# Optimization experiments

Hardware: AMD Instinct MI355X
Metric: run time of the kernel (lower is better)

The kernel has to match this reference:

```python
import jax, jax.numpy as jnp
import numpy as np

EPS = 1e-6

def _mlp3(x, Wa, ba, Wb, bb, Wc, bc):
    h = jax.nn.relu(x @ Wa + ba)
    h = jax.nn.relu(h @ Wb + bb)
    return h @ Wc + bc

def setup_inputs() -> dict:
    key = jax.random.key(0)
    ks = jax.random.split(key, 16)
    B, D, C, N = 1024, 1024, 128, 100000
    s = 0.02  # weight scale
    return {
        "query": jax.random.normal(ks[0], (B, D), jnp.float32),
        "W1": jax.random.normal(ks[1], (D, D // 2), jnp.float32) * s,
        "b1": jnp.zeros((D // 2,), jnp.float32),
        "W2": jax.random.normal(ks[2], (D // 2, D // 4), jnp.float32) * s,
        "b2": jnp.zeros((D // 4,), jnp.float32),
        "W3": jax.random.normal(ks[3], (D // 4, C), jnp.float32) * s,
        "b3": jnp.zeros((C,), jnp.float32),
        "keys": jax.random.normal(ks[4], (N, C), jnp.float32),
        "values": jax.random.normal(ks[5], (N, C), jnp.float32),
        "D1w": jax.random.normal(ks[6], (C, D // 4), jnp.float32) * s,
        "D1b": jnp.zeros((D // 4,), jnp.float32),
        "D2w": jax.random.normal(ks[7], (D // 4, D // 2), jnp.float32) * s,
        "D2b": jnp.zeros((D // 2,), jnp.float32),
        "D3w": jax.random.normal(ks[8], (D // 2, D), jnp.float32) * s,
        "D3b": jnp.zeros((D,), jnp.float32),
        "k": 5,
    }

def reference(query, W1, b1, W2, b2, W3, b3, keys, values,
              D1w, D1b, D2w, D2b, D3w, D3b, k):
    # Compress query (FAISS path detaches, so stop_gradient is faithful)
    cq = _mlp3(query, W1, b1, W2, b2, W3, b3)          # [B, C]
    cq = jax.lax.stop_gradient(cq)
    keys_c = jax.lax.stop_gradient(keys)
    vals = jax.lax.stop_gradient(values)               # stored values were .detach()ed
    # Brute-force squared-L2 distances (IndexFlatL2 returns squared L2): [B, N]
    d2 = (jnp.sum(cq * cq, axis=1, keepdims=True)
          + jnp.sum(keys_c * keys_c, axis=1)[None, :]
          - 2.0 * cq @ keys_c.T)
    neg_d, idx = jax.lax.top_k(-d2, k)                 # k nearest, ascending distance
    dist = -neg_d                                      # [B, k]
    w = 1.0 / (dist + EPS)
    w = w / jnp.sum(w, axis=1, keepdims=True)          # [B, k]
    gathered = vals[idx]                               # [B, k, C]
    weighted = jnp.einsum('bk,bkc->bc', w, gathered)   # [B, C]
    retrieved = _mlp3(weighted, D1w, D1b, D2w, D2b, D3w, D3b)  # [B, D]
    confidence = 1.0 / (dist[:, 0] + EPS)              # [B]
    return retrieved, confidence
```

## Files before the change

### kernel.cpp

```cpp
#include <hip/hip_runtime.h>
#include <hip/hip_bf16.h>

#define NKEYS  100000
#define NCH    192
#define CHK    576
#define TPC    9
#define KPAD   (NCH * CHK)
#define NTILE  (KPAD / 64)
#define BQ     1024
#define EPS_F  1e-6f
#define NCAND  (NCH * 3)
#define BIGF   1e30f

typedef __attribute__((ext_vector_type(8))) short bf16x8;
typedef __attribute__((ext_vector_type(4))) float f32x4;

__device__ __forceinline__ void gl_lds16(const uint4* g, uint4* l) {
    __builtin_amdgcn_global_load_lds((const __attribute__((address_space(1))) void*)g,
                                     (__attribute__((address_space(3))) void*)l, 16, 0, 0);
}
__device__ __forceinline__ unsigned umn(unsigned a, unsigned b) { return a < b ? a : b; }
__device__ __forceinline__ unsigned umx(unsigned a, unsigned b) { return a > b ? a : b; }
__device__ __forceinline__ ushort bf16bits(float v) {
    __hip_bfloat16 h = __float2bfloat16(v);
    return *(ushort*)&h;
}

__device__ __forceinline__ void ins3u(unsigned (&m)[3], unsigned u) {
    unsigned v1 = umn(m[2], u);
    m[2] = umx(m[1], v1);
    unsigned v2 = umn(m[1], v1);
    m[1] = umx(m[0], v2);
    m[0] = umn(m[0], v2);
}

__device__ __forceinline__ void ins5(float (&d)[5], int (&ix)[5], float nd, int ni) {
    if (nd < d[4]) {
        d[4] = nd; ix[4] = ni;
#pragma unroll
        for (int p = 4; p > 0; --p) {
            if (d[p] < d[p - 1]) {
                float td = d[p]; d[p] = d[p - 1]; d[p - 1] = td;
                int   ti = ix[p]; ix[p] = ix[p - 1]; ix[p - 1] = ti;
            }
        }
    }
}

__global__ __launch_bounds__(256)
void cvt_keys(const float* __restrict__ keys, uint4* __restrict__ img,
              float* __restrict__ kk, float* __restrict__ khalf) {
    const int tid = threadIdx.x;
    const int r = tid >> 2, s = tid & 3;
    const int tile = blockIdx.x;
    const int n = tile * 64 + r;
    const int ct = r >> 4, l15 = r & 15;
    const bool live = (n < NKEYS);
    const float* kp = keys + (size_t)n * 128 + s * 32;
    float ss = 0.f;
    uint4 out[4];
#pragma unroll
    for (int q = 0; q < 4; ++q) {
        float4 a = make_float4(0.f, 0.f, 0.f, 0.f), b = a;
        if (live) { a = *(const float4*)(kp + q * 8); b = *(const float4*)(kp + q * 8 + 4); }
        ss += a.x * a.x + a.y * a.y + a.z * a.z + a.w * a.w
            + b.x * b.x + b.y * b.y + b.z * b.z + b.w * b.w;
        float v[8] = {a.x, a.y, a.z, a.w, b.x, b.y, b.z, b.w};
        ushort h[8];
#pragma unroll
        for (int j = 0; j < 8; ++j) h[j] = bf16bits(v[j]);
        out[q] = make_uint4((uint)h[0] | ((uint)h[1] << 16), (uint)h[2] | ((uint)h[3] << 16),
                            (uint)h[4] | ((uint)h[5] << 16), (uint)h[6] | ((uint)h[7] << 16));
    }
    ss += __shfl_xor(ss, 1, 64);
    ss += __shfl_xor(ss, 2, 64);
    if (s == 0) {
        kk[n]    = live ? ss : BIGF;
        khalf[n] = live ? -0.5f * ss : -BIGF;
    }
#pragma unroll
    for (int q = 0; q < 4; ++q)
        img[(size_t)tile * 1024 + ((ct * 4 + s) * 4 + q) * 16 + l15] = out[q];
}

__global__ __launch_bounds__(256)
void prep(const float* __restrict__ A, ushort* __restrict__ Ax,
          const float* __restrict__ W, uint4* __restrict__ Wimg) {
    const int b = blockIdx.x;
    if (b < 1024) {
        const int row = b;
        const int i = threadIdx.x * 4;
        float4 v = *(const float4*)&A[(size_t)row * 1024 + i];
        float x[4] = {v.x, v.y, v.z, v.w};
        ushort h[4], l[4];
#pragma unroll
        for (int j = 0; j < 4; ++j) {
            __hip_bfloat16 hb = __float2bfloat16(x[j]);
            h[j] = *(ushort*)&hb;
            l[j] = bf16bits(x[j] - __bfloat162float(hb));
        }
        ushort* o = Ax + (size_t)row * 3072;
        *(ushort4*)&o[i]        = make_ushort4(h[0], h[1], h[2], h[3]);
        *(ushort4*)&o[1024 + i] = make_ushort4(l[0], l[1], l[2], l[3]);
        *(ushort4*)&o[2048 + i] = make_ushort4(h[0], h[1], h[2], h[3]);
    } else {
        const int idx = b - 1024;
        const int ctile = idx / 48, p = idx % 48;
        const int part = p >> 4, psrc = p & 15;
#pragma unroll
        for (int it = 0; it < 2; ++it) {
            int c = it * 256 + threadIdx.x;
            int l15 = c & 15, quad = (c >> 4) & 3, s = (c >> 6) & 1, ct = c >> 7;
            int n = ctile * 64 + ct * 16 + l15;
            int k = psrc * 64 + s * 32 + quad * 8;
            ushort h[8];
#pragma unroll
            for (int j = 0; j < 8; ++j) {
                float w = W[(size_t)(k + j) * 512 + n];
                __hip_bfloat16 hb = __float2bfloat16(w);
                if (part < 2) h[j] = *(ushort*)&hb;
                else h[j] = bf16bits(w - __bfloat162float(hb));
            }
            Wimg[((size_t)ctile * 48 + p) * 512 + c] =
                make_uint4((uint)h[0] | ((uint)h[1] << 16), (uint)h[2] | ((uint)h[3] << 16),
                           (uint)h[4] | ((uint)h[5] << 16), (uint)h[6] | ((uint)h[7] << 16));
        }
    }
}

__global__ __launch_bounds__(256)
void bgemm_part(const ushort* __restrict__ Abf, const uint4* __restrict__ Wimg,
                float* __restrict__ P, int M, int N, int K, int ppz) {
    __shared__ uint4 pan[2][512];
    const int tid = threadIdx.x;
    const int wv = tid >> 6, ln = tid & 63;
    const int quad = ln >> 4, l15 = ln & 15;
    const int n0 = blockIdx.x * 64;
    const int m0 = blockIdx.y * 128 + wv * 32;
    const int ctile = blockIdx.x, npanT = K >> 6;
    const int p0 = blockIdx.z * ppz;
    f32x4 acc[2][4];
#pragma unroll
    for (int s = 0; s < 2; ++s)
#pragma unroll
        for (int c = 0; c < 4; ++c) acc[s][c] = (f32x4){0.f, 0.f, 0.f, 0.f};

#pragma unroll
    for (int it = 0; it < 2; ++it)
        gl_lds16(&Wimg[((size_t)ctile * npanT + p0) * 512 + it * 256 + wv * 64 + ln],
                 &pan[0][it * 256 + wv * 64]);
    __syncthreads();

    for (int pp = 0; pp < ppz; ++pp) {
        const int p = p0 + pp;
        const int b = pp & 1;
        if (pp + 1 < ppz) {
#pragma unroll
            for (int it = 0; it < 2; ++it)
                gl_lds16(&Wimg[((size_t)ctile * npanT + p + 1) * 512 + it * 256 + wv * 64 + ln],
                         &pan[b ^ 1][it * 256 + wv * 64]);
        }
        const ushort* arow = Abf + (size_t)(m0 + l15) * K + p * 64 + quad * 8;
        bf16x8 afA[2], afB[2];
#pragma unroll
        for (int s = 0; s < 2; ++s) {
            afA[s] = *(const bf16x8*)(arow + s * 32);
            afB[s] = *(const bf16x8*)(arow + (size_t)16 * K + s * 32);
        }
#pragma unroll
        for (int ct = 0; ct < 4; ++ct)
#pragma unroll
            for (int s = 0; s < 2; ++s) {
                bf16x8 bfr = *(const bf16x8*)&pan[b][((ct * 2 + s) * 4 + quad) * 16 + l15];
                acc[0][ct] = __builtin_amdgcn_mfma_f32_16x16x32_bf16(afA[s], bfr, acc[0][ct], 0, 0, 0);
                acc[1][ct] = __builtin_amdgcn_mfma_f32_16x16x32_bf16(afB[s], bfr, acc[1][ct], 0, 0, 0);
            }
        __syncthreads();
    }

    P += (size_t)blockIdx.z * M * N;
#pragma unroll
    for (int ct = 0; ct < 4; ++ct) {
        const int col = n0 + ct * 16 + l15;
#pragma unroll
        for (int set = 0; set < 2; ++set)
#pragma unroll
            for (int r = 0; r < 4; ++r)
                P[(size_t)(m0 + set * 16 + quad * 4 + r) * N + col] = acc[set][ct][r];
    }
}

template <int NP>
__global__ __launch_bounds__(256)
void sgemm_part(const float* __restrict__ A, const float* __restrict__ abias,
                const float* __restrict__ W, float* __restrict__ P,
                int M, int N, int K, int kslice, int MNpart) {
    __shared__ float As[16][68];
    __shared__ float Bs[16][64];
    const int tid = threadIdx.x;
    const int tx = tid & 15, ty = tid >> 4;
    const int m0 = blockIdx.y * 64, n0 = blockIdx.x * 64;
    const int kb = blockIdx.z * kslice, ke = kb + kslice;
    float acc[4][4] = {};
    for (int k0 = kb; k0 < ke; k0 += 16) {
        {
            int m = tid >> 2, k4 = (tid & 3) * 4;
            const float* ap = &A[(size_t)(m0 + m) * K + k0 + k4];
            float4 a = *(const float4*)ap;
            if (NP > 0) {
#pragma unroll
                for (int z = 1; z < NP; ++z) {
                    float4 v = *(const float4*)(ap + (size_t)z * MNpart);
                    a.x += v.x; a.y += v.y; a.z += v.z; a.w += v.w;
                }
                float4 b = *(const float4*)&abias[k0 + k4];
                a.x = fmaxf(a.x + b.x, 0.f); a.y = fmaxf(a.y + b.y, 0.f);
                a.z = fmaxf(a.z + b.z, 0.f); a.w = fmaxf(a.w + b.w, 0.f);
            }
            As[k4 + 0][m] = a.x; As[k4 + 1][m] = a.y;
            As[k4 + 2][m] = a.z; As[k4 + 3][m] = a.w;
        }
        {
            int k = tid >> 4, n4 = (tid & 15) * 4;
            *(float4*)&Bs[k][n4] = *(const float4*)&W[(size_t)(k0 + k) * N + n0 + n4];
        }
        __syncthreads();
#pragma unroll
        for (int kkk = 0; kkk < 16; ++kkk) {
            float4 a4 = *(const float4*)&As[kkk][ty * 4];
            float4 b4 = *(const float4*)&Bs[kkk][tx * 4];
            float av[4] = {a4.x, a4.y, a4.z, a4.w};
            float bv[4] = {b4.x, b4.y, b4.z, b4.w};
#pragma unroll
            for (int i = 0; i < 4; ++i)
#pragma unroll
                for (int j = 0; j < 4; ++j)
                    acc[i][j] = fmaf(av[i], bv[j], acc[i][j]);
        }
        __syncthreads();
    }
    P += (size_t)blockIdx.z * M * N;
#pragma unroll
    for (int i = 0; i < 4; ++i)
        *(float4*)&P[(size_t)(m0 + ty * 4 + i) * N + n0 + tx * 4] =
            make_float4(acc[i][0], acc[i][1], acc[i][2], acc[i][3]);
}

__global__ __launch_bounds__(128)
void final_row(const float* __restrict__ P, const float* __restrict__ bias,
               float* __restrict__ cq, ushort* __restrict__ qbf,
               float* __restrict__ qq) {
    __shared__ float red[2];
    const int row = blockIdx.x, c = threadIdx.x;
    float v = 0.f;
#pragma unroll
    for (int z = 0; z < 4; ++z) v += P[(size_t)z * (BQ * 128) + row * 128 + c];
    v += bias[c];
    cq[(size_t)row * 128 + c] = v;
    qbf[(size_t)row * 128 + c] = bf16bits(v);
    float s = v * v;
#pragma unroll
    for (int off = 32; off > 0; off >>= 1) s += __shfl_down(s, off, 64);
    if ((c & 63) == 0) red[c >> 6] = s;
    __syncthreads();
    if (c == 0) qq[row] = red[0] + red[1];
}

__device__ __forceinline__ void wT_panel(const float* __restrict__ W, uint4* __restrict__ Wimg,
                                         int K, int N, int ctile, int p) {
    const int npan = K >> 6;
#pragma unroll
    for (int it = 0; it < 2; ++it) {
        int c = it * 256 + threadIdx.x;
        int l15 = c & 15, quad = (c >> 4) & 3, s = (c >> 6) & 1, ct = c >> 7;
        int n = ctile * 64 + ct * 16 + l15;
        int k = p * 64 + s * 32 + quad * 8;
        ushort h[8];
#pragma unroll
        for (int j = 0; j < 8; ++j) h[j] = bf16bits(W[(size_t)(k + j) * N + n]);
        Wimg[((size_t)ctile * npan + p) * 512 + c] =
            make_uint4((uint)h[0] | ((uint)h[1] << 16), (uint)h[2] | ((uint)h[3] << 16),
                       (uint)h[4] | ((uint)h[5] << 16), (uint)h[6] | ((uint)h[7] << 16));
    }
}

__global__ __launch_bounds__(256)
void cvt_wT_all(const float* __restrict__ W1, const float* __restrict__ W2,
                const float* __restrict__ W3, uint4* __restrict__ I1,
                uint4* __restrict__ I2, uint4* __restrict__ I3) {
    int b = blockIdx.x;
    if (b < 8)       { wT_panel(W1, I1, 128, 256,  b >> 1, b & 1); }
    else if (b < 40) { b -= 8;  wT_panel(W2, I2, 256, 512,  b >> 2, b & 3); }
    else             { b -= 40; wT_panel(W3, I3, 512, 1024, b >> 3, b & 7); }
}

__global__ __launch_bounds__(512, 4)
void screen_topk(const ushort* __restrict__ qbf, const uint4* __restrict__ img,
                 const float* __restrict__ khalf, int* __restrict__ cand_i) {
    __shared__ uint4 buf[2][1024];
    __shared__ float kls[CHK];
    const int tid = threadIdx.x;
    const int wv = tid >> 6, ln = tid & 63;
    const int quad = ln >> 4, l15 = ln & 15;
    const int m0 = blockIdx.y * 256 + wv * 32;
    const int c0 = blockIdx.x * CHK;
    const int t0 = blockIdx.x * TPC;

    bf16x8 afA[4], afB[4];
    {
        const ushort* qa = qbf + (size_t)(m0 + l15) * 128 + quad * 8;
#pragma unroll
        for (int s = 0; s < 4; ++s) {
            afA[s] = *(const bf16x8*)(qa + 32 * s);
            afB[s] = *(const bf16x8*)(qa + 16 * 128 + 32 * s);
        }
    }
    for (int i = tid; i < CHK; i += 512) kls[i] = khalf[c0 + i];

    unsigned mA[4][3], mB[4][3];
#pragma unroll
    for (int r = 0; r < 4; ++r)
#pragma unroll
        for (int p = 0; p < 3; ++p) { mA[r][p] = 0xFFFFFFFFu; mB[r][p] = 0xFFFFFFFFu; }

#pragma unroll
    for (int it = 0; it < 2; ++it)
        gl_lds16(&img[(size_t)t0 * 1024 + it * 512 + wv * 64 + ln],
                 &buf[0][it * 512 + wv * 64]);
    __syncthreads();

    for (int t = 0; t < TPC; ++t) {
        const int b = t & 1;
        if (t + 1 < TPC) {
#pragma unroll
            for (int it = 0; it < 2; ++it)
                gl_lds16(&img[(size_t)(t0 + t + 1) * 1024 + it * 512 + wv * 64 + ln],
                         &buf[b ^ 1][it * 512 + wv * 64]);
        }
#pragma unroll
        for (int ct = 0; ct < 4; ++ct) {
            const int nl = t * 64 + ct * 16 + l15;
            const float kh = kls[nl];
            f32x4 a0 = {kh, kh, kh, kh}, a1 = {kh, kh, kh, kh};
#pragma unroll
            for (int s = 0; s < 4; ++s) {
                bf16x8 bfr = *(const bf16x8*)&buf[b][(ct * 4 + s) * 64 + ln];
                a0 = __builtin_amdgcn_mfma_f32_16x16x32_bf16(afA[s], bfr, a0, 0, 0, 0);
                a1 = __builtin_amdgcn_mfma_f32_16x16x32_bf16(afB[s], bfr, a1, 0, 0, 0);
            }
#pragma unroll
            for (int r = 0; r < 4; ++r) {
                ins3u(mA[r], (__float_as_uint(a0[r]) & 0xFFFFF800u) | (unsigned)nl);
                ins3u(mB[r], (__float_as_uint(a1[r]) & 0xFFFFF800u) | (unsigned)nl);
            }
        }
        __syncthreads();
    }

#pragma unroll
    for (int set = 0; set < 2; ++set) {
#pragma unroll
        for (int r = 0; r < 4; ++r) {
            unsigned m[3];
#pragma unroll
            for (int p = 0; p < 3; ++p) m[p] = set ? mB[r][p] : mA[r][p];
#pragma unroll
            for (int st = 1; st <= 8; st <<= 1) {
                unsigned o[3];
#pragma unroll
                for (int p = 0; p < 3; ++p) o[p] = (unsigned)__shfl_xor((int)m[p], st, 64);
#pragma unroll
                for (int p = 0; p < 3; ++p) ins3u(m, o[p]);
            }
            if (l15 == 0) {
                const int row = m0 + set * 16 + quad * 4 + r;
#pragma unroll
                for (int p = 0; p < 3; ++p)
                    cand_i[((size_t)row * NCH + blockIdx.x) * 3 + p] = c0 + (int)(m[p] & 0x7FFu);
            }
        }
    }
}

__global__ __launch_bounds__(512)
void rerank_gather(const int* __restrict__ cand_i, const float* __restrict__ cq,
                   const float* __restrict__ keysf, const float* __restrict__ qq,
                   const float* __restrict__ kk, const float* __restrict__ values,
                   ushort* __restrict__ wbf, float* __restrict__ conf_out) {
    __shared__ __align__(16) float qs[128];
    __shared__ float ed[NCAND];
    __shared__ int   ei[NCAND];
    __shared__ float w5[5];
    __shared__ int   s5[5];
    __shared__ float confs;
    const int row = blockIdx.x, tid = threadIdx.x;
    const int ln = tid & 63;
    const int qd = tid >> 4;
    const int l15 = tid & 15;
    if (tid < 128) qs[tid] = cq[(size_t)row * 128 + tid];
    for (int c = tid; c < NCAND; c += 512) ei[c] = cand_i[(size_t)row * NCAND + c];
    __syncthreads();
    const float4 qa = *(const float4*)&qs[l15 * 8];
    const float4 qb = *(const float4*)&qs[l15 * 8 + 4];
    const float qqr = qq[row];
#pragma unroll 3
    for (int it = 0; it < (NCAND + 31) / 32; ++it) {
        const int c = qd + it * 32;
        if (c < NCAND) {
            const int idx = ei[c];
            const int idc = idx < NKEYS ? idx : NKEYS - 1;
            const float* kp = &keysf[(size_t)idc * 128 + l15 * 8];
            const float4 ka = *(const float4*)kp;
            const float4 kb = *(const float4*)(kp + 4);
            float dot = qa.x * ka.x + qa.y * ka.y + qa.z * ka.z + qa.w * ka.w
                      + qb.x * kb.x + qb.y * kb.y + qb.z * kb.z + qb.w * kb.w;
            dot += __shfl_xor(dot, 1, 64);
            dot += __shfl_xor(dot, 2, 64);
            dot += __shfl_xor(dot, 4, 64);
            dot += __shfl_xor(dot, 8, 64);
            if (l15 == 0) ed[c] = qqr + kk[idx] - 2.0f * dot;
        }
    }
    __syncthreads();
    if (tid < 64) {
        float bd[5]; int bi[5];
#pragma unroll
        for (int p = 0; p < 5; ++p) { bd[p] = BIGF; bi[p] = 0; }
        for (int c = ln; c < NCAND; c += 64) ins5(bd, bi, ed[c], ei[c]);
#pragma unroll
        for (int m = 1; m <= 32; m <<= 1) {
            float od[5]; int oi[5];
#pragma unroll
            for (int p = 0; p < 5; ++p) {
                od[p] = __shfl_xor(bd[p], m, 64);
                oi[p] = __shfl_xor(bi[p], m, 64);
            }
#pragma unroll
            for (int p = 0; p < 5; ++p) ins5(bd, bi, od[p], oi[p]);
        }
        if (ln == 0) {
            float ww[5]; float s = 0.f;
#pragma unroll
            for (int p = 0; p < 5; ++p) { ww[p] = 1.0f / (bd[p] + EPS_F); s += ww[p]; }
#pragma unroll
            for (int p = 0; p < 5; ++p) { w5[p] = ww[p] / s; s5[p] = bi[p]; }
            confs = 1.0f / (bd[0] + EPS_F);
        }
    }
    __syncthreads();
    if (tid < 128) {
        float acc = 0.f;
#pragma unroll
        for (int p = 0; p < 5; ++p) acc += w5[p] * values[(size_t)s5[p] * 128 + tid];
        wbf[(size_t)row * 128 + tid] = bf16bits(acc);
    }
    if (tid == 0) conf_out[row] = confs;
}

template <int RELU, int OUTF32>
__global__ __launch_bounds__(256)
void bgemm_bias(const ushort* __restrict__ Abf, const uint4* __restrict__ Wimg,
                const float* __restrict__ bias, void* __restrict__ Cout,
                int M, int N, int K) {
    __shared__ uint4 pan[2][512];
    const int tid = threadIdx.x;
    const int wv = tid >> 6, ln = tid & 63;
    const int quad = ln >> 4, l15 = ln & 15;
    const int n0 = blockIdx.x * 64;
    const int m0 = blockIdx.y * 128 + wv * 32;
    const int ctile = blockIdx.x, npan = K >> 6;
    f32x4 acc[2][4];
#pragma unroll
    for (int s = 0; s < 2; ++s)
#pragma unroll
        for (int c = 0; c < 4; ++c) acc[s][c] = (f32x4){0.f, 0.f, 0.f, 0.f};

#pragma unroll
    for (int it = 0; it < 2; ++it)
        gl_lds16(&Wimg[(size_t)ctile * npan * 512 + it * 256 + wv * 64 + ln],
                 &pan[0][it * 256 + wv * 64]);
    __syncthreads();

    for (int p = 0; p < npan; ++p) {
        const int b = p & 1;
        if (p + 1 < npan) {
#pragma unroll
            for (int it = 0; it < 2; ++it)
                gl_lds16(&Wimg[((size_t)ctile * npan + p + 1) * 512 + it * 256 + wv * 64 + ln],
                         &pan[b ^ 1][it * 256 + wv * 64]);
        }
        const ushort* arow = Abf + (size_t)(m0 + l15) * K + p * 64 + quad * 8;
        bf16x8 afA[2], afB[2];
#pragma unroll
        for (int s = 0; s < 2; ++s) {
            afA[s] = *(const bf16x8*)(arow + s * 32);
            afB[s] = *(const bf16x8*)(arow + (size_t)16 * K + s * 32);
        }
#pragma unroll
        for (int ct = 0; ct < 4; ++ct)
#pragma unroll
            for (int s = 0; s < 2; ++s) {
                bf16x8 bfr = *(const bf16x8*)&pan[b][((ct * 2 + s) * 4 + quad) * 16 + l15];
                acc[0][ct] = __builtin_amdgcn_mfma_f32_16x16x32_bf16(afA[s], bfr, acc[0][ct], 0, 0, 0);
                acc[1][ct] = __builtin_amdgcn_mfma_f32_16x16x32_bf16(afB[s], bfr, acc[1][ct], 0, 0, 0);
            }
        __syncthreads();
    }

#pragma unroll
    for (int ct = 0; ct < 4; ++ct) {
        const int col = n0 + ct * 16 + l15;
        const float bv = bias[col];
#pragma unroll
        for (int set = 0; set < 2; ++set)
#pragma unroll
            for (int r = 0; r < 4; ++r) {
                float v = acc[set][ct][r] + bv;
                if (RELU) v = fmaxf(v, 0.f);
                const int row = m0 + set * 16 + quad * 4 + r;
                if (OUTF32) ((float*)Cout)[(size_t)row * N + col] = v;
                else        ((ushort*)Cout)[(size_t)row * N + col] = bf16bits(v);
            }
    }
}

extern "C" void kernel_launch(void* const* d_in, const int* in_sizes, int n_in,
                              void* d_out, int out_size, void* d_ws, size_t ws_size,
                              hipStream_t stream) {
    const float* query  = (const float*)d_in[0];
    const float* W1     = (const float*)d_in[1];
    const float* b1     = (const float*)d_in[2];
    const float* W2     = (const float*)d_in[3];
    const float* b2     = (const float*)d_in[4];
    const float* W3     = (const float*)d_in[5];
    const float* b3     = (const float*)d_in[6];
    const float* keys   = (const float*)d_in[7];
    const float* values = (const float*)d_in[8];
    const float* D1w    = (const float*)d_in[9];
    const float* D1b    = (const float*)d_in[10];
    const float* D2w    = (const float*)d_in[11];
    const float* D2b    = (const float*)d_in[12];
    const float* D3w    = (const float*)d_in[13];
    const float* D3b    = (const float*)d_in[14];
    float* out = (float*)d_out;

    float*  ws    = (float*)d_ws;
    float*  kk    = ws;
    float*  khalf = ws + 110592;
    float*  qq    = ws + 221184;
    float*  cq    = ws + 222208;
    ushort* qbf   = (ushort*)(ws + 353280);
    int*    cand  = (int*)(ws + 418816);
    float*  R     = ws + 1008640;
    ushort* xbig  = (ushort*)R;
    uint4*  W1img = (uint4*)(R + 1572864);
    float*  partA = R + 2359296;
    float*  partB = R + 5505024;
    float*  partC = R + 6553600;
    uint4*  img   = (uint4*)R;
    ushort* wbf   = (ushort*)R;
    ushort* h3bf  = (ushort*)(R + 65536);
    ushort* h4bf  = (ushort*)(R + 196608);
    uint4*  Wimg1 = (uint4*)(R + 458752);
    uint4*  Wimg2 = (uint4*)(R + 475136);
    uint4*  Wimg3 = (uint4*)(R + 540672);
    float*  conf  = out + 1024 * 1024;

    prep<<<1408, 256, 0, stream>>>(query, xbig, W1, W1img);
    bgemm_part<<<dim3(8, 8, 6), 256, 0, stream>>>(xbig, W1img, partA, 1024, 512, 3072, 8);
    sgemm_part<6><<<dim3(4, 16, 4), 256, 0, stream>>>(partA, b1, W2, partB, 1024, 256, 512, 128, 1024 * 512);
    sgemm_part<4><<<dim3(2, 16, 4), 256, 0, stream>>>(partB, b2, W3, partC, 1024, 128, 256, 64, 1024 * 256);
    final_row<<<1024, 128, 0, stream>>>(partC, b3, cq, qbf, qq);
    cvt_keys<<<NTILE, 256, 0, stream>>>(keys, img, kk, khalf);
    screen_topk<<<dim3(NCH, BQ / 256), 512, 0, stream>>>(qbf, img, khalf, cand);
    rerank_gather<<<BQ, 512, 0, stream>>>(cand, cq, keys, qq, kk, values, wbf, conf);
    cvt_wT_all<<<168, 256, 0, stream>>>(D1w, D2w, D3w, Wimg1, Wimg2, Wimg3);
    bgemm_bias<1, 0><<<dim3(4, 8),  256, 0, stream>>>(wbf,  Wimg1, D1b, h3bf, 1024, 256,  128);
    bgemm_bias<1, 0><<<dim3(8, 8),  256, 0, stream>>>(h3bf, Wimg2, D2b, h4bf, 1024, 512,  256);
    bgemm_bias<0, 1><<<dim3(16, 8), 256, 0, stream>>>(h4bf, Wimg3, D3b, out,  1024, 1024, 512);

    (void)in_sizes; (void)n_in; (void)out_size; (void)ws_size;
}
```

Before: 295.1 us.

## Fuse layer-3 GEMM with row finalize, merge weight conversion, rechunk key screening

Replaces the split-K third encoder GEMM and its row-reduction kernel with one per-row kernel that reduces layer-2 partials, applies ReLU, multiplies by W3 and emits cq, bf16 query and norms. The decoder weight conversion is folded into the key-conversion launch as extra blocks. The screening chunk layout changes from 192 chunks of 576 keys to 128 chunks of 832, and the workspace is relaid so the weight images no longer alias the reused region. Together these remove two launches and an intermediate buffer, with fewer, larger screening blocks. The cost is that the fused layer-3 kernel does a naive per-row dot product that rereads W3 from global memory for every row.

After: 283.3 us. 4.0% less time.

```diff
diff --git a/kernel.cpp b/kernel.cpp
--- a/kernel.cpp
+++ b/kernel.cpp
@@ -2,9 +2,9 @@
 #include <hip/hip_bf16.h>
 
 #define NKEYS  100000
-#define NCH    192
-#define CHK    576
-#define TPC    9
+#define NCH    128
+#define CHK    832
+#define TPC    13
 #define KPAD   (NCH * CHK)
 #define NTILE  (KPAD / 64)
 #define BQ     1024
@@ -47,9 +47,37 @@
     }
 }
 
+__device__ __forceinline__ void wT_panel(const float* __restrict__ W, uint4* __restrict__ Wimg,
+                                         int K, int N, int ctile, int p) {
+    const int npan = K >> 6;
+#pragma unroll
+    for (int it = 0; it < 2; ++it) {
+        int c = it * 256 + threadIdx.x;
+        int l15 = c & 15, quad = (c >> 4) & 3, s = (c >> 6) & 1, ct = c >> 7;
+        int n = ctile * 64 + ct * 16 + l15;
+        int k = p * 64 + s * 32 + quad * 8;
+        ushort h[8];
+#pragma unroll
+        for (int j = 0; j < 8; ++j) h[j] = bf16bits(W[(size_t)(k + j) * N + n]);
+        Wimg[((size_t)ctile * npan + p) * 512 + c] =
+            make_uint4((uint)h[0] | ((uint)h[1] << 16), (uint)h[2] | ((uint)h[3] << 16),
+                       (uint)h[4] | ((uint)h[5] << 16), (uint)h[6] | ((uint)h[7] << 16));
+    }
+}
+
 __global__ __launch_bounds__(256)
-void cvt_keys(const float* __restrict__ keys, uint4* __restrict__ img,
-              float* __restrict__ kk, float* __restrict__ khalf) {
+void cvt_keys_w(const float* __restrict__ keys, uint4* __restrict__ img,
+                float* __restrict__ kk, float* __restrict__ khalf,
+                const float* __restrict__ D1w, const float* __restrict__ D2w,
+                const float* __restrict__ D3w, uint4* __restrict__ I1,
+                uint4* __restrict__ I2, uint4* __restrict__ I3) {
+    if (blockIdx.x >= NTILE) {
+        int b = blockIdx.x - NTILE;
+        if (b < 8)       { wT_panel(D1w, I1, 128, 256,  b >> 1, b & 1); }
+        else if (b < 40) { b -= 8;  wT_panel(D2w, I2, 256, 512,  b >> 2, b & 3); }
+        else             { b -= 40; wT_panel(D3w, I3, 512, 1024, b >> 3, b & 7); }
+        return;
+    }
     const int tid = threadIdx.x;
     const int r = tid >> 2, s = tid & 3;
     const int tile = blockIdx.x;
@@ -247,51 +275,39 @@
 }
 
 __global__ __launch_bounds__(128)
-void final_row(const float* __restrict__ P, const float* __restrict__ bias,
-               float* __restrict__ cq, ushort* __restrict__ qbf,
-               float* __restrict__ qq) {
+void layer3_full(const float* __restrict__ partB, const float* __restrict__ b2,
+                 const float* __restrict__ W3, const float* __restrict__ b3,
+                 float* __restrict__ cq, ushort* __restrict__ qbf,
+                 float* __restrict__ qq) {
+    __shared__ float h2s[256];
     __shared__ float red[2];
     const int row = blockIdx.x, c = threadIdx.x;
-    float v = 0.f;
-#pragma unroll
-    for (int z = 0; z < 4; ++z) v += P[(size_t)z * (BQ * 128) + row * 128 + c];
-    v += bias[c];
-    cq[(size_t)row * 128 + c] = v;
-    qbf[(size_t)row * 128 + c] = bf16bits(v);
-    float s = v * v;
+#pragma unroll
+    for (int u = 0; u < 2; ++u) {
+        const int k = c + u * 128;
+        float v = 0.f;
+#pragma unroll
+        for (int z = 0; z < 4; ++z) v += partB[(size_t)z * (BQ * 256) + row * 256 + k];
+        h2s[k] = fmaxf(v + b2[k], 0.f);
+    }
+    __syncthreads();
+    float a0 = 0.f, a1 = 0.f, a2 = 0.f, a3 = 0.f;
+#pragma unroll 4
+    for (int k = 0; k < 256; k += 4) {
+        a0 = fmaf(h2s[k + 0], W3[(size_t)(k + 0) * 128 + c], a0);
+        a1 = fmaf(h2s[k + 1], W3[(size_t)(k + 1) * 128 + c], a1);
+        a2 = fmaf(h2s[k + 2], W3[(size_t)(k + 2) * 128 + c], a2);
+        a3 = fmaf(h2s[k + 3], W3[(size_t)(k + 3) * 128 + c], a3);
+    }
+    const float out = (a0 + a1) + (a2 + a3) + b3[c];
+    cq[(size_t)row * 128 + c] = out;
+    qbf[(size_t)row * 128 + c] = bf16bits(out);
+    float s = out * out;
 #pragma unroll
     for (int off = 32; off > 0; off >>= 1) s += __shfl_down(s, off, 64);
     if ((c & 63) == 0) red[c >> 6] = s;
     __syncthreads();
     if (c == 0) qq[row] = red[0] + red[1];
-}
-
-__device__ __forceinline__ void wT_panel(const float* __restrict__ W, uint4* __restrict__ Wimg,
-                                         int K, int N, int ctile, int p) {
-    const int npan = K >> 6;
-#pragma unroll
-    for (int it = 0; it < 2; ++it) {
-        int c = it * 256 + threadIdx.x;
-        int l15 = c & 15, quad = (c >> 4) & 3, s = (c >> 6) & 1, ct = c >> 7;
-        int n = ctile * 64 + ct * 16 + l15;
-        int k = p * 64 + s * 32 + quad * 8;
-        ushort h[8];
-#pragma unroll
-        for (int j = 0; j < 8; ++j) h[j] = bf16bits(W[(size_t)(k + j) * N + n]);
-        Wimg[((size_t)ctile * npan + p) * 512 + c] =
-            make_uint4((uint)h[0] | ((uint)h[1] << 16), (uint)h[2] | ((uint)h[3] << 16),
-                       (uint)h[4] | ((uint)h[5] << 16), (uint)h[6] | ((uint)h[7] << 16));
-    }
-}
-
-__global__ __launch_bounds__(256)
-void cvt_wT_all(const float* __restrict__ W1, const float* __restrict__ W2,
-                const float* __restrict__ W3, uint4* __restrict__ I1,
-                uint4* __restrict__ I2, uint4* __restrict__ I3) {
-    int b = blockIdx.x;
-    if (b < 8)       { wT_panel(W1, I1, 128, 256,  b >> 1, b & 1); }
-    else if (b < 40) { b -= 8;  wT_panel(W2, I2, 256, 512,  b >> 2, b & 3); }
-    else             { b -= 40; wT_panel(W3, I3, 512, 1024, b >> 3, b & 7); }
 }
 
 __global__ __launch_bounds__(512, 4)
@@ -546,35 +562,33 @@
 
     float*  ws    = (float*)d_ws;
     float*  kk    = ws;
-    float*  khalf = ws + 110592;
-    float*  qq    = ws + 221184;
-    float*  cq    = ws + 222208;
-    ushort* qbf   = (ushort*)(ws + 353280);
-    int*    cand  = (int*)(ws + 418816);
-    float*  R     = ws + 1008640;
+    float*  khalf = ws + 106496;
+    float*  qq    = ws + 212992;
+    float*  cq    = ws + 214016;
+    ushort* qbf   = (ushort*)(ws + 345088);
+    int*    cand  = (int*)(ws + 410624);
+    uint4*  Wimg1 = (uint4*)(ws + 803840);
+    uint4*  Wimg2 = (uint4*)(ws + 820224);
+    uint4*  Wimg3 = (uint4*)(ws + 885760);
+    float*  R     = ws + 1147904;
     ushort* xbig  = (ushort*)R;
     uint4*  W1img = (uint4*)(R + 1572864);
     float*  partA = R + 2359296;
     float*  partB = R + 5505024;
-    float*  partC = R + 6553600;
     uint4*  img   = (uint4*)R;
     ushort* wbf   = (ushort*)R;
     ushort* h3bf  = (ushort*)(R + 65536);
     ushort* h4bf  = (ushort*)(R + 196608);
-    uint4*  Wimg1 = (uint4*)(R + 458752);
-    uint4*  Wimg2 = (uint4*)(R + 475136);
-    uint4*  Wimg3 = (uint4*)(R + 540672);
     float*  conf  = out + 1024 * 1024;
 
     prep<<<1408, 256, 0, stream>>>(query, xbig, W1, W1img);
     bgemm_part<<<dim3(8, 8, 6), 256, 0, stream>>>(xbig, W1img, partA, 1024, 512, 3072, 8);
     sgemm_part<6><<<dim3(4, 16, 4), 256, 0, stream>>>(partA, b1, W2, partB, 1024, 256, 512, 128, 1024 * 512);
-    sgemm_part<4><<<dim3(2, 16, 4), 256, 0, stream>>>(partB, b2, W3, partC, 1024, 128, 256, 64, 1024 * 256);
-    final_row<<<1024, 128, 0, stream>>>(partC, b3, cq, qbf, qq);
-    cvt_keys<<<NTILE, 256, 0, stream>>>(keys, img, kk, khalf);
+    layer3_full<<<1024, 128, 0, stream>>>(partB, b2, W3, b3, cq, qbf, qq);
+    cvt_keys_w<<<NTILE + 168, 256, 0, stream>>>(keys, img, kk, khalf,
+                                                D1w, D2w, D3w, Wimg1, Wimg2, Wimg3);
     screen_topk<<<dim3(NCH, BQ / 256), 512, 0, stream>>>(qbf, img, khalf, cand);
     rerank_gather<<<BQ, 512, 0, stream>>>(cand, cq, keys, qq, kk, values, wbf, conf);
-    cvt_wT_all<<<168, 256, 0, stream>>>(D1w, D2w, D3w, Wimg1, Wimg2, Wimg3);
     bgemm_bias<1, 0><<<dim3(4, 8),  256, 0, stream>>>(wbf,  Wimg1, D1b, h3bf, 1024, 256,  128);
     bgemm_bias<1, 0><<<dim3(8, 8),  256, 0, stream>>>(h3bf, Wimg2, D2b, h4bf, 1024, 512,  256);
     bgemm_bias<0, 1><<<dim3(16, 8), 256, 0, stream>>>(h4bf, Wimg3, D3b, out,  1024, 1024, 512);
```
